# Optimization experiments

Hardware: AMD Instinct MI355X
Metric: run time of the kernel (lower is better)

The kernel has to match this reference:

```python
import jax, jax.numpy as jnp
import numpy as np

B, T, F = 4096, 256, 20
VOCAB, EMB = 1281, 4
UNITS = (64, 32, 32, 32)


def setup_inputs() -> dict:
    key = jax.random.key(0)
    ks = jax.random.split(key, 16)
    feats = jax.random.normal(ks[0], (B, T, F), jnp.float32)
    ids = jax.random.randint(ks[1], (B, T), 0, VOCAB).astype(jnp.float32)
    input_tensor = feats.at[:, :, 1].set(ids)  # column 1 = org ids
    W_emb = jax.random.normal(ks[2], (VOCAB, EMB), jnp.float32) * 0.1
    in_dims = (F - 2 + 1 + EMB,) + UNITS[:-1]  # (23, 64, 32, 32)
    out = {"input_tensor": input_tensor, "W_emb": W_emb}
    for i, (din, u) in enumerate(zip(in_dims, UNITS)):
        out[f"k{i}"] = jax.random.normal(ks[3 + 3 * i], (din, 3 * u), jnp.float32) * 0.1
        out[f"rk{i}"] = jax.random.normal(ks[4 + 3 * i], (u, 3 * u), jnp.float32) * 0.1
        out[f"b{i}"] = jnp.zeros((2, 3 * u), jnp.float32)  # [input_bias, recurrent_bias] (reset_after)
    out["Wd"] = jax.random.normal(ks[15], (UNITS[-1], 2), jnp.float32) * 0.1
    out["bd"] = jnp.zeros((2,), jnp.float32)
    return out


def _gru(h, x, k, rk, b):
    # Keras GRUCell, reset_after=True (TF2 default)
    mx = x @ k + b[0]
    mh = h @ rk + b[1]
    xz, xr, xh = jnp.split(mx, 3, axis=-1)
    hz, hr, hh = jnp.split(mh, 3, axis=-1)
    z = jax.nn.sigmoid(xz + hz)
    r = jax.nn.sigmoid(xr + hr)
    hc = jnp.tanh(xh + r * hh)
    return z * h + (1.0 - z) * hc


def reference(input_tensor, W_emb, k0, rk0, b0, k1, rk1, b1, k2, rk2, b2, k3, rk3, b3, Wd, bd):
    f0 = input_tensor[:, :, :1]                      # [B,T,1]
    ids = input_tensor[:, :, 1].astype(jnp.int32)    # [B,T]
    rest = input_tensor[:, :, 2:]                    # [B,T,F-2]
    emb = W_emb[ids]                                 # [B,T,EMB]
    x = jnp.concatenate([f0, rest, emb], axis=-1)    # [B,T,F+3]
    xs = jnp.swapaxes(x, 0, 1)                       # [T,B,F+3]
    bsz = x.shape[0]
    h_init = tuple(jnp.zeros((bsz, u), x.dtype) for u in UNITS)
    layer_params = ((k0, rk0, b0), (k1, rk1, b1), (k2, rk2, b2), (k3, rk3, b3))

    def step(carry, xt):
        hs = []
        inp = xt
        for h, (k, rk, b) in zip(carry, layer_params):
            h = _gru(h, inp, k, rk, b)
            hs.append(h)
            inp = h
        return tuple(hs), None

    hs, _ = jax.lax.scan(step, h_init, xs)
    # return_sequences + [:, -1, :] == final hidden state of last layer
    logits = hs[-1] @ Wd + bd
    return jax.nn.softmax(logits, axis=-1)
```

## Files before the change

kernel.cpp:

```cpp
#include <hip/hip_runtime.h>


typedef __attribute__((ext_vector_type(8))) __bf16 bf16x8;
typedef __attribute__((ext_vector_type(4))) float f32x4;

#define TT 256
#define FF 20
#define BT 16
#define CH 64
#define SH0 72
#define SH1 40
#define XSTR 648

__device__ __forceinline__ f32x4 mfma16(bf16x8 a, bf16x8 b, f32x4 c) {
  return __builtin_amdgcn_mfma_f32_16x16x32_bf16(a, b, c, 0, 0, 0);
}

__device__ __forceinline__ float sigm(float x) {
  return __builtin_amdgcn_rcpf(1.f + __builtin_amdgcn_exp2f(-1.44269504f * x));
}
__device__ __forceinline__ float tanh_(float x) {
  return __builtin_amdgcn_rcpf(1.f + __builtin_amdgcn_exp2f(-2.88539008f * x)) * 2.f - 1.f;
}

__device__ __forceinline__ bf16x8 bfragW(const float* W, int Kreal, int N,
                                         int ncol, int kbase) {
  bf16x8 r;
#pragma unroll
  for (int j = 0; j < 8; ++j) {
    int k = kbase + j;
    r[j] = (__bf16)(k < Kreal ? W[k * N + ncol] : 0.f);
  }
  return r;
}

__device__ __forceinline__ bf16x8 afrag(const __bf16* base, int stride, int m,
                                        int kbase) {
  return *(const bf16x8*)(base + m * stride + kbase);
}

__device__ __forceinline__ void gates(f32x4 az, f32x4 ar, f32x4 axh, f32x4 ahh,
                                      float* h, __bf16* dst, int stride, int rowq) {
#pragma unroll
  for (int r = 0; r < 4; ++r) {
    float z  = sigm(az[r]);
    float rg = sigm(ar[r]);
    float hc = tanh_(fmaf(rg, ahh[r], axh[r]));
    float hn = fmaf(z, h[r] - hc, hc);
    h[r] = hn;
    dst[(rowq + r) * stride] = (__bf16)hn;
  }
}

extern "C" __global__ void __launch_bounds__(512, 2)
gru4(const float* __restrict__ inp, const float* __restrict__ Wemb,
     const float* __restrict__ k0, const float* __restrict__ rk0, const float* __restrict__ b0,
     const float* __restrict__ k1, const float* __restrict__ rk1, const float* __restrict__ b1,
     const float* __restrict__ k2, const float* __restrict__ rk2, const float* __restrict__ b2,
     const float* __restrict__ k3, const float* __restrict__ rk3, const float* __restrict__ b3,
     const float* __restrict__ Wd, const float* __restrict__ bd,
     float* __restrict__ out)
{
  __shared__ __align__(16) __bf16 x_ch[CH * XSTR];
  __shared__ __align__(16) __bf16 h0_lds[2][BT * SH0];
  __shared__ __align__(16) __bf16 h1_lds[2][BT * SH1];
  __shared__ __align__(16) __bf16 h2_lds[2][BT * SH1];
  __shared__ __align__(16) __bf16 h3_lds[2][BT * SH1];
  __shared__ __align__(16) float h3f[BT * 32];

  const int tid  = threadIdx.x;
  const int lane = tid & 63;
  const int w    = tid >> 6;
  const int col  = lane & 15;
  const int kb   = (lane >> 4) * 8;
  const int rowq = (lane >> 4) * 4;
  const long bbase = (long)blockIdx.x * BT;
  const float* binp = inp + bbase * TT * FF;

  bf16x8 z0x, r0x, g0x, z0h0, z0h1, r0h0, r0h1, g0h0, g0h1;
  float bz0 = 0, br0 = 0, bxh0 = 0, bhh0 = 0;
  if (w < 4) {
    int u = w * 16 + col;
    z0x  = bfragW(k0, 23, 192, u, kb);
    r0x  = bfragW(k0, 23, 192, 64 + u, kb);
    g0x  = bfragW(k0, 23, 192, 128 + u, kb);
    z0h0 = bfragW(rk0, 64, 192, u, kb);
    z0h1 = bfragW(rk0, 64, 192, u, 32 + kb);
    r0h0 = bfragW(rk0, 64, 192, 64 + u, kb);
    r0h1 = bfragW(rk0, 64, 192, 64 + u, 32 + kb);
    g0h0 = bfragW(rk0, 64, 192, 128 + u, kb);
    g0h1 = bfragW(rk0, 64, 192, 128 + u, 32 + kb);
    bz0  = b0[u] + b0[192 + u];
    br0  = b0[64 + u] + b0[192 + 64 + u];
    bxh0 = b0[128 + u];
    bhh0 = b0[192 + 128 + u];
  }

  bf16x8 z1x0, z1x1, r1x0, r1x1, g1x0, g1x1, z1h, r1h, g1h;
  float bz1 = 0, br1 = 0, bxh1 = 0, bhh1 = 0;
  if (w == 4 || w == 5) {
    int u = (w - 4) * 16 + col;
    z1x0 = bfragW(k1, 64, 96, u, kb);
    z1x1 = bfragW(k1, 64, 96, u, 32 + kb);
    r1x0 = bfragW(k1, 64, 96, 32 + u, kb);
    r1x1 = bfragW(k1, 64, 96, 32 + u, 32 + kb);
    g1x0 = bfragW(k1, 64, 96, 64 + u, kb);
    g1x1 = bfragW(k1, 64, 96, 64 + u, 32 + kb);
    z1h  = bfragW(rk1, 32, 96, u, kb);
    r1h  = bfragW(rk1, 32, 96, 32 + u, kb);
    g1h  = bfragW(rk1, 32, 96, 64 + u, kb);
    bz1  = b1[u] + b1[96 + u];
    br1  = b1[32 + u] + b1[96 + 32 + u];
    bxh1 = b1[64 + u];
    bhh1 = b1[96 + 64 + u];
  }

  bf16x8 z2x, r2x, g2x, z2h, r2h, g2h;
  bf16x8 z3x, r3x, g3x, z3h, r3h, g3h;
  float bz2 = 0, br2 = 0, bxh2 = 0, bhh2 = 0;
  float bz3 = 0, br3 = 0, bxh3 = 0, bhh3 = 0;
  if (w >= 6) {
    int u = (w - 6) * 16 + col;
    z2x = bfragW(k2, 32, 96, u, kb);
    r2x = bfragW(k2, 32, 96, 32 + u, kb);
    g2x = bfragW(k2, 32, 96, 64 + u, kb);
    z2h = bfragW(rk2, 32, 96, u, kb);
    r2h = bfragW(rk2, 32, 96, 32 + u, kb);
    g2h = bfragW(rk2, 32, 96, 64 + u, kb);
    bz2  = b2[u] + b2[96 + u];
    br2  = b2[32 + u] + b2[96 + 32 + u];
    bxh2 = b2[64 + u];
    bhh2 = b2[96 + 64 + u];
    z3x = bfragW(k3, 32, 96, u, kb);
    r3x = bfragW(k3, 32, 96, 32 + u, kb);
    g3x = bfragW(k3, 32, 96, 64 + u, kb);
    z3h = bfragW(rk3, 32, 96, u, kb);
    r3h = bfragW(rk3, 32, 96, 32 + u, kb);
    g3h = bfragW(rk3, 32, 96, 64 + u, kb);
    bz3  = b3[u] + b3[96 + u];
    br3  = b3[32 + u] + b3[96 + 32 + u];
    bxh3 = b3[64 + u];
    bhh3 = b3[96 + 64 + u];
  }

  {
    __bf16* p0 = (__bf16*)h0_lds;
    for (int i = tid; i < 2 * BT * SH0; i += 512) p0[i] = (__bf16)0.f;
    __bf16* p1 = (__bf16*)h1_lds;
    __bf16* p2 = (__bf16*)h2_lds;
    __bf16* p3 = (__bf16*)h3_lds;
    for (int i = tid; i < 2 * BT * SH1; i += 512) {
      p1[i] = (__bf16)0.f; p2[i] = (__bf16)0.f; p3[i] = (__bf16)0.f;
    }
  }
  float h0r[4] = {0,0,0,0}, h1r[4] = {0,0,0,0};
  float h2r[4] = {0,0,0,0}, h3r[4] = {0,0,0,0};
  __syncthreads();

  for (int s = 0; s < TT + 3; ++s) {
    if ((s & (CH - 1)) == 0 && s < TT) {
      const int row = tid >> 5;
      const int tg  = (tid & 31) * 2;
      const float* rp = binp + ((long)row * TT + s + tg) * FF;
#pragma unroll
      for (int tt = 0; tt < 2; ++tt) {
        const float* p = rp + tt * FF;
        float4 v0 = *(const float4*)(p);
        float4 v1 = *(const float4*)(p + 4);
        float4 v2 = *(const float4*)(p + 8);
        float4 v3 = *(const float4*)(p + 12);
        float4 v4 = *(const float4*)(p + 16);
        float4 e  = *(const float4*)(Wemb + 4 * (int)v0.y);
        __bf16* d = &x_ch[(tg + tt) * XSTR + row * 40];
        bf16x8 q0 = {(__bf16)v0.x, (__bf16)v0.z, (__bf16)v0.w, (__bf16)v1.x,
                     (__bf16)v1.y, (__bf16)v1.z, (__bf16)v1.w, (__bf16)v2.x};
        bf16x8 q1 = {(__bf16)v2.y, (__bf16)v2.z, (__bf16)v2.w, (__bf16)v3.x,
                     (__bf16)v3.y, (__bf16)v3.z, (__bf16)v3.w, (__bf16)v4.x};
        bf16x8 q2 = {(__bf16)v4.y, (__bf16)v4.z, (__bf16)v4.w, (__bf16)e.x,
                     (__bf16)e.y,  (__bf16)e.z,  (__bf16)e.w,  (__bf16)0.f};
        bf16x8 q3 = {(__bf16)0.f, (__bf16)0.f, (__bf16)0.f, (__bf16)0.f,
                     (__bf16)0.f, (__bf16)0.f, (__bf16)0.f, (__bf16)0.f};
        *(bf16x8*)(d)      = q0;
        *(bf16x8*)(d + 8)  = q1;
        *(bf16x8*)(d + 16) = q2;
        *(bf16x8*)(d + 24) = q3;
      }
      __syncthreads();
    }

    const int pb = (s + 1) & 1;
    const int qb = s & 1;

    if (w < 4) {
      if (s < TT) {
        const int tl = s & (CH - 1);
        bf16x8 ax = *(const bf16x8*)(&x_ch[tl * XSTR + col * 40 + kb]);
        bf16x8 a0 = afrag(h0_lds[pb], SH0, col, kb);
        bf16x8 a1 = afrag(h0_lds[pb], SH0, col, 32 + kb);
        f32x4 az  = {bz0, bz0, bz0, bz0};
        f32x4 ar  = {br0, br0, br0, br0};
        f32x4 axh = {bxh0, bxh0, bxh0, bxh0};
        f32x4 ahh = {bhh0, bhh0, bhh0, bhh0};
        az  = mfma16(ax, z0x, az);  az  = mfma16(a0, z0h0, az);  az = mfma16(a1, z0h1, az);
        ar  = mfma16(ax, r0x, ar);  ar  = mfma16(a0, r0h0, ar);  ar = mfma16(a1, r0h1, ar);
        axh = mfma16(ax, g0x, axh);
        ahh = mfma16(a0, g0h0, ahh); ahh = mfma16(a1, g0h1, ahh);
        gates(az, ar, axh, ahh, h0r, &h0_lds[qb][w * 16 + col], SH0, rowq);
      }
    } else if (w < 6) {
      if (s >= 1 && s <= TT) {
        bf16x8 ax0 = afrag(h0_lds[pb], SH0, col, kb);
        bf16x8 ax1 = afrag(h0_lds[pb], SH0, col, 32 + kb);
        bf16x8 ah  = afrag(h1_lds[pb], SH1, col, kb);
        f32x4 az  = {bz1, bz1, bz1, bz1};
        f32x4 ar  = {br1, br1, br1, br1};
        f32x4 axh = {bxh1, bxh1, bxh1, bxh1};
        f32x4 ahh = {bhh1, bhh1, bhh1, bhh1};
        az  = mfma16(ax0, z1x0, az);  az  = mfma16(ax1, z1x1, az);  az = mfma16(ah, z1h, az);
        ar  = mfma16(ax0, r1x0, ar);  ar  = mfma16(ax1, r1x1, ar);  ar = mfma16(ah, r1h, ar);
        axh = mfma16(ax0, g1x0, axh); axh = mfma16(ax1, g1x1, axh);
        ahh = mfma16(ah, g1h, ahh);
        gates(az, ar, axh, ahh, h1r, &h1_lds[qb][(w - 4) * 16 + col], SH1, rowq);
      }
    } else {
      bf16x8 a1 = afrag(h1_lds[pb], SH1, col, kb);
      bf16x8 a2 = afrag(h2_lds[pb], SH1, col, kb);
      bf16x8 a3 = afrag(h3_lds[pb], SH1, col, kb);
      if (s >= 2 && s <= TT + 1) {
        f32x4 az  = {bz2, bz2, bz2, bz2};
        f32x4 ar  = {br2, br2, br2, br2};
        f32x4 axh = {bxh2, bxh2, bxh2, bxh2};
        f32x4 ahh = {bhh2, bhh2, bhh2, bhh2};
        az  = mfma16(a1, z2x, az);  az = mfma16(a2, z2h, az);
        ar  = mfma16(a1, r2x, ar);  ar = mfma16(a2, r2h, ar);
        axh = mfma16(a1, g2x, axh);
        ahh = mfma16(a2, g2h, ahh);
        gates(az, ar, axh, ahh, h2r, &h2_lds[qb][(w - 6) * 16 + col], SH1, rowq);
      }
      if (s >= 3) {
        f32x4 az  = {bz3, bz3, bz3, bz3};
        f32x4 ar  = {br3, br3, br3, br3};
        f32x4 axh = {bxh3, bxh3, bxh3, bxh3};
        f32x4 ahh = {bhh3, bhh3, bhh3, bhh3};
        az  = mfma16(a2, z3x, az);  az = mfma16(a3, z3h, az);
        ar  = mfma16(a2, r3x, ar);  ar = mfma16(a3, r3h, ar);
        axh = mfma16(a2, g3x, axh);
        ahh = mfma16(a3, g3h, ahh);
        gates(az, ar, axh, ahh, h3r, &h3_lds[qb][(w - 6) * 16 + col], SH1, rowq);
      }
    }

    __syncthreads();
  }

  if (w >= 6) {
#pragma unroll
    for (int r = 0; r < 4; ++r)
      h3f[(rowq + r) * 32 + (w - 6) * 16 + col] = h3r[r];
  }
  __syncthreads();

  if (tid < BT) {
    float l0 = bd[0], l1 = bd[1];
#pragma unroll
    for (int u = 0; u < 32; ++u) {
      float h = h3f[tid * 32 + u];
      l0 = fmaf(h, Wd[2 * u], l0);
      l1 = fmaf(h, Wd[2 * u + 1], l1);
    }
    float m = fmaxf(l0, l1);
    float e0 = __builtin_amdgcn_exp2f((l0 - m) * 1.44269504f);
    float e1 = __builtin_amdgcn_exp2f((l1 - m) * 1.44269504f);
    float inv = 1.f / (e0 + e1);
    out[(bbase + tid) * 2 + 0] = e0 * inv;
    out[(bbase + tid) * 2 + 1] = e1 * inv;
  }
}

extern "C" void kernel_launch(void* const* d_in, const int* in_sizes, int n_in,
                              void* d_out, int out_size, void* d_ws, size_t ws_size,
                              hipStream_t stream) {
  const float* inp  = (const float*)d_in[0];
  const float* Wemb = (const float*)d_in[1];
  const float* k0   = (const float*)d_in[2];
  const float* rk0  = (const float*)d_in[3];
  const float* b0   = (const float*)d_in[4];
  const float* k1   = (const float*)d_in[5];
  const float* rk1  = (const float*)d_in[6];
  const float* b1   = (const float*)d_in[7];
  const float* k2   = (const float*)d_in[8];
  const float* rk2  = (const float*)d_in[9];
  const float* b2   = (const float*)d_in[10];
  const float* k3   = (const float*)d_in[11];
  const float* rk3  = (const float*)d_in[12];
  const float* b3   = (const float*)d_in[13];
  const float* Wd   = (const float*)d_in[14];
  const float* bd   = (const float*)d_in[15];
  float* out = (float*)d_out;

  const int Btot = in_sizes[0] / (TT * FF);
  dim3 grid(Btot / BT);
  gru4<<<grid, 512, 0, stream>>>(inp, Wemb, k0, rk0, b0, k1, rk1, b1,
                                 k2, rk2, b2, k3, rk3, b3, Wd, bd, out);
}
```

Baseline: 365.6 us.

## Rebalance GRU layer work across twelve waves with uniform per-wave step code

Grows the block from 8 to 12 waves. Layers 2 and 3 now get their own waves instead of one wave doing both, and layer 0 is split across six waves: some duplicate the MFMA work and each computes only half of the gate rows. Every wave runs the same generic MFMA plus gate sequence, chosen by per-wave pointers and flags, which shortens the longest wave's critical path per timestep. The cost is more waves per block, a changed occupancy target (launch bounds 768 threads, 3 blocks), redundant MFMAs on the layer-0 waves, and branchy generic code with possibly wasted zero-weight MFMAs.

```diff
diff --git a/kernel.cpp b/kernel.cpp
--- a/kernel.cpp
+++ b/kernel.cpp
@@ -11,6 +11,7 @@
 #define SH0 72
 #define SH1 40
 #define XSTR 648
+#define NTHR 768
 
 __device__ __forceinline__ f32x4 mfma16(bf16x8 a, bf16x8 b, f32x4 c) {
   return __builtin_amdgcn_mfma_f32_16x16x32_bf16(a, b, c, 0, 0, 0);
@@ -34,25 +35,7 @@
   return r;
 }
 
-__device__ __forceinline__ bf16x8 afrag(const __bf16* base, int stride, int m,
-                                        int kbase) {
-  return *(const bf16x8*)(base + m * stride + kbase);
-}
-
-__device__ __forceinline__ void gates(f32x4 az, f32x4 ar, f32x4 axh, f32x4 ahh,
-                                      float* h, __bf16* dst, int stride, int rowq) {
-#pragma unroll
-  for (int r = 0; r < 4; ++r) {
-    float z  = sigm(az[r]);
-    float rg = sigm(ar[r]);
-    float hc = tanh_(fmaf(rg, ahh[r], axh[r]));
-    float hn = fmaf(z, h[r] - hc, hc);
-    h[r] = hn;
-    dst[(rowq + r) * stride] = (__bf16)hn;
-  }
-}
-
-extern "C" __global__ void __launch_bounds__(512, 2)
+extern "C" __global__ void __launch_bounds__(NTHR, 3)
 gru4(const float* __restrict__ inp, const float* __restrict__ Wemb,
      const float* __restrict__ k0, const float* __restrict__ rk0, const float* __restrict__ b0,
      const float* __restrict__ k1, const float* __restrict__ rk1, const float* __restrict__ b1,
@@ -77,186 +60,192 @@
   const long bbase = (long)blockIdx.x * BT;
   const float* binp = inp + bbase * TT * FF;
 
-  bf16x8 z0x, r0x, g0x, z0h0, z0h1, r0h0, r0h1, g0h0, g0h1;
-  float bz0 = 0, br0 = 0, bxh0 = 0, bhh0 = 0;
-  if (w < 4) {
-    int u = w * 16 + col;
-    z0x  = bfragW(k0, 23, 192, u, kb);
-    r0x  = bfragW(k0, 23, 192, 64 + u, kb);
-    g0x  = bfragW(k0, 23, 192, 128 + u, kb);
-    z0h0 = bfragW(rk0, 64, 192, u, kb);
-    z0h1 = bfragW(rk0, 64, 192, u, 32 + kb);
-    r0h0 = bfragW(rk0, 64, 192, 64 + u, kb);
-    r0h1 = bfragW(rk0, 64, 192, 64 + u, 32 + kb);
-    g0h0 = bfragW(rk0, 64, 192, 128 + u, kb);
-    g0h1 = bfragW(rk0, 64, 192, 128 + u, 32 + kb);
-    bz0  = b0[u] + b0[192 + u];
-    br0  = b0[64 + u] + b0[192 + 64 + u];
-    bxh0 = b0[128 + u];
-    bhh0 = b0[192 + 128 + u];
-  }
-
-  bf16x8 z1x0, z1x1, r1x0, r1x1, g1x0, g1x1, z1h, r1h, g1h;
-  float bz1 = 0, br1 = 0, bxh1 = 0, bhh1 = 0;
-  if (w == 4 || w == 5) {
-    int u = (w - 4) * 16 + col;
-    z1x0 = bfragW(k1, 64, 96, u, kb);
-    z1x1 = bfragW(k1, 64, 96, u, 32 + kb);
-    r1x0 = bfragW(k1, 64, 96, 32 + u, kb);
-    r1x1 = bfragW(k1, 64, 96, 32 + u, 32 + kb);
-    g1x0 = bfragW(k1, 64, 96, 64 + u, kb);
-    g1x1 = bfragW(k1, 64, 96, 64 + u, 32 + kb);
-    z1h  = bfragW(rk1, 32, 96, u, kb);
-    r1h  = bfragW(rk1, 32, 96, 32 + u, kb);
-    g1h  = bfragW(rk1, 32, 96, 64 + u, kb);
-    bz1  = b1[u] + b1[96 + u];
-    br1  = b1[32 + u] + b1[96 + 32 + u];
-    bxh1 = b1[64 + u];
-    bhh1 = b1[96 + 64 + u];
-  }
-
-  bf16x8 z2x, r2x, g2x, z2h, r2h, g2h;
-  bf16x8 z3x, r3x, g3x, z3h, r3h, g3h;
-  float bz2 = 0, br2 = 0, bxh2 = 0, bhh2 = 0;
-  float bz3 = 0, br3 = 0, bxh3 = 0, bhh3 = 0;
-  if (w >= 6) {
-    int u = (w - 6) * 16 + col;
-    z2x = bfragW(k2, 32, 96, u, kb);
-    r2x = bfragW(k2, 32, 96, 32 + u, kb);
-    g2x = bfragW(k2, 32, 96, 64 + u, kb);
-    z2h = bfragW(rk2, 32, 96, u, kb);
-    r2h = bfragW(rk2, 32, 96, 32 + u, kb);
-    g2h = bfragW(rk2, 32, 96, 64 + u, kb);
-    bz2  = b2[u] + b2[96 + u];
-    br2  = b2[32 + u] + b2[96 + 32 + u];
-    bxh2 = b2[64 + u];
-    bhh2 = b2[96 + 64 + u];
-    z3x = bfragW(k3, 32, 96, u, kb);
-    r3x = bfragW(k3, 32, 96, 32 + u, kb);
-    g3x = bfragW(k3, 32, 96, 64 + u, kb);
-    z3h = bfragW(rk3, 32, 96, u, kb);
-    r3h = bfragW(rk3, 32, 96, 32 + u, kb);
-    g3h = bfragW(rk3, 32, 96, 64 + u, kb);
-    bz3  = b3[u] + b3[96 + u];
-    br3  = b3[32 + u] + b3[96 + 32 + u];
-    bxh3 = b3[64 + u];
-    bhh3 = b3[96 + 64 + u];
-  }
+  bf16x8 zf;
+#pragma unroll
+  for (int j = 0; j < 8; ++j) zf[j] = (__bf16)0.f;
+
+  bf16x8 Wz0 = zf, Wz1 = zf, Wz2 = zf;
+  bf16x8 Wr0 = zf, Wr1 = zf, Wr2 = zf;
+  bf16x8 Wgx0 = zf, Wgx1 = zf, Wgx2 = zf;
+  bf16x8 Wgh0 = zf, Wgh1 = zf, Wgh2 = zf;
+  float bz = 0.f, br = 0.f, bxh = 0.f, bhh = 0.f;
+  const __bf16 *A0b = x_ch, *A1b = x_ch, *A2b = x_ch;
+  int D0 = 0, D1 = 0, D2 = 0;
+  __bf16* Wwr0 = (__bf16*)h3f;
+  int WD = 0, wstride = SH1;
+  int lay = 0;
+  bool doLo = false, doHi = false, threeA = false;
+
+  if (w < 6) {
+    lay = 0; threeA = true;
+    const int sl = (w < 4) ? (w >> 1) : (w - 2);
+    doLo = (w >= 4) || ((w & 1) == 0);
+    doHi = (w >= 4) || ((w & 1) == 1);
+    const int u = sl * 16 + col;
+    Wz0 = bfragW(k0, 23, 192, u, kb);
+    Wz1 = bfragW(rk0, 64, 192, u, kb);
+    Wz2 = bfragW(rk0, 64, 192, u, 32 + kb);
+    Wr0 = bfragW(k0, 23, 192, 64 + u, kb);
+    Wr1 = bfragW(rk0, 64, 192, 64 + u, kb);
+    Wr2 = bfragW(rk0, 64, 192, 64 + u, 32 + kb);
+    Wgx0 = bfragW(k0, 23, 192, 128 + u, kb);
+    Wgh1 = bfragW(rk0, 64, 192, 128 + u, kb);
+    Wgh2 = bfragW(rk0, 64, 192, 128 + u, 32 + kb);
+    bz  = b0[u] + b0[192 + u];
+    br  = b0[64 + u] + b0[192 + 64 + u];
+    bxh = b0[128 + u];
+    bhh = b0[192 + 128 + u];
+    A1b = &h0_lds[0][col * SH0 + kb];      D1 = BT * SH0;
+    A2b = &h0_lds[0][col * SH0 + 32 + kb]; D2 = BT * SH0;
+    Wwr0 = &h0_lds[0][rowq * SH0 + sl * 16 + col];
+    WD = BT * SH0; wstride = SH0;
+  } else if (w < 8) {
+    lay = 1; threeA = true; doLo = doHi = true;
+    const int u = (w - 6) * 16 + col;
+    Wz0 = bfragW(k1, 64, 96, u, kb);
+    Wz1 = bfragW(k1, 64, 96, u, 32 + kb);
+    Wz2 = bfragW(rk1, 32, 96, u, kb);
+    Wr0 = bfragW(k1, 64, 96, 32 + u, kb);
+    Wr1 = bfragW(k1, 64, 96, 32 + u, 32 + kb);
+    Wr2 = bfragW(rk1, 32, 96, 32 + u, kb);
+    Wgx0 = bfragW(k1, 64, 96, 64 + u, kb);
+    Wgx1 = bfragW(k1, 64, 96, 64 + u, 32 + kb);
+    Wgh2 = bfragW(rk1, 32, 96, 64 + u, kb);
+    bz  = b1[u] + b1[96 + u];
+    br  = b1[32 + u] + b1[96 + 32 + u];
+    bxh = b1[64 + u];
+    bhh = b1[96 + 64 + u];
+    A0b = &h0_lds[0][col * SH0 + kb];      D0 = BT * SH0;
+    A1b = &h0_lds[0][col * SH0 + 32 + kb]; D1 = BT * SH0;
+    A2b = &h1_lds[0][col * SH1 + kb];      D2 = BT * SH1;
+    Wwr0 = &h1_lds[0][rowq * SH1 + (w - 6) * 16 + col];
+    WD = BT * SH1; wstride = SH1;
+  } else if (w < 10) {
+    lay = 2; threeA = false; doLo = doHi = true;
+    const int u = (w - 8) * 16 + col;
+    Wz0 = bfragW(k2, 32, 96, u, kb);
+    Wz1 = bfragW(rk2, 32, 96, u, kb);
+    Wr0 = bfragW(k2, 32, 96, 32 + u, kb);
+    Wr1 = bfragW(rk2, 32, 96, 32 + u, kb);
+    Wgx0 = bfragW(k2, 32, 96, 64 + u, kb);
+    Wgh1 = bfragW(rk2, 32, 96, 64 + u, kb);
+    bz  = b2[u] + b2[96 + u];
+    br  = b2[32 + u] + b2[96 + 32 + u];
+    bxh = b2[64 + u];
+    bhh = b2[96 + 64 + u];
+    A0b = &h1_lds[0][col * SH1 + kb]; D0 = BT * SH1;
+    A1b = &h2_lds[0][col * SH1 + kb]; D1 = BT * SH1;
+    A2b = A1b; D2 = D1;
+    Wwr0 = &h2_lds[0][rowq * SH1 + (w - 8) * 16 + col];
+    WD = BT * SH1; wstride = SH1;
+  } else {
+    lay = 3; threeA = false; doLo = doHi = true;
+    const int u = (w - 10) * 16 + col;
+    Wz0 = bfragW(k3, 32, 96, u, kb);
+    Wz1 = bfragW(rk3, 32, 96, u, kb);
+    Wr0 = bfragW(k3, 32, 96, 32 + u, kb);
+    Wr1 = bfragW(rk3, 32, 96, 32 + u, kb);
+    Wgx0 = bfragW(k3, 32, 96, 64 + u, kb);
+    Wgh1 = bfragW(rk3, 32, 96, 64 + u, kb);
+    bz  = b3[u] + b3[96 + u];
+    br  = b3[32 + u] + b3[96 + 32 + u];
+    bxh = b3[64 + u];
+    bhh = b3[96 + 64 + u];
+    A0b = &h2_lds[0][col * SH1 + kb]; D0 = BT * SH1;
+    A1b = &h3_lds[0][col * SH1 + kb]; D1 = BT * SH1;
+    A2b = A1b; D2 = D1;
+    Wwr0 = &h3_lds[0][rowq * SH1 + (w - 10) * 16 + col];
+    WD = BT * SH1; wstride = SH1;
+  }
+
+  const __bf16* xb = &x_ch[col * 40 + kb];
 
   {
     __bf16* p0 = (__bf16*)h0_lds;
-    for (int i = tid; i < 2 * BT * SH0; i += 512) p0[i] = (__bf16)0.f;
+    for (int i = tid; i < 2 * BT * SH0; i += NTHR) p0[i] = (__bf16)0.f;
     __bf16* p1 = (__bf16*)h1_lds;
     __bf16* p2 = (__bf16*)h2_lds;
     __bf16* p3 = (__bf16*)h3_lds;
-    for (int i = tid; i < 2 * BT * SH1; i += 512) {
+    for (int i = tid; i < 2 * BT * SH1; i += NTHR) {
       p1[i] = (__bf16)0.f; p2[i] = (__bf16)0.f; p3[i] = (__bf16)0.f;
     }
   }
-  float h0r[4] = {0,0,0,0}, h1r[4] = {0,0,0,0};
-  float h2r[4] = {0,0,0,0}, h3r[4] = {0,0,0,0};
+  float hreg[4] = {0.f, 0.f, 0.f, 0.f};
   __syncthreads();
 
   for (int s = 0; s < TT + 3; ++s) {
     if ((s & (CH - 1)) == 0 && s < TT) {
-      const int row = tid >> 5;
-      const int tg  = (tid & 31) * 2;
-      const float* rp = binp + ((long)row * TT + s + tg) * FF;
-#pragma unroll
-      for (int tt = 0; tt < 2; ++tt) {
-        const float* p = rp + tt * FF;
+      for (int idx = tid; idx < BT * CH; idx += NTHR) {
+        const int row = idx >> 6;
+        const int tg  = idx & (CH - 1);
+        const float* p = binp + ((long)row * TT + s + tg) * FF;
         float4 v0 = *(const float4*)(p);
         float4 v1 = *(const float4*)(p + 4);
         float4 v2 = *(const float4*)(p + 8);
         float4 v3 = *(const float4*)(p + 12);
         float4 v4 = *(const float4*)(p + 16);
         float4 e  = *(const float4*)(Wemb + 4 * (int)v0.y);
-        __bf16* d = &x_ch[(tg + tt) * XSTR + row * 40];
+        __bf16* d = &x_ch[tg * XSTR + row * 40];
         bf16x8 q0 = {(__bf16)v0.x, (__bf16)v0.z, (__bf16)v0.w, (__bf16)v1.x,
                      (__bf16)v1.y, (__bf16)v1.z, (__bf16)v1.w, (__bf16)v2.x};
         bf16x8 q1 = {(__bf16)v2.y, (__bf16)v2.z, (__bf16)v2.w, (__bf16)v3.x,
                      (__bf16)v3.y, (__bf16)v3.z, (__bf16)v3.w, (__bf16)v4.x};
         bf16x8 q2 = {(__bf16)v4.y, (__bf16)v4.z, (__bf16)v4.w, (__bf16)e.x,
                      (__bf16)e.y,  (__bf16)e.z,  (__bf16)e.w,  (__bf16)0.f};
-        bf16x8 q3 = {(__bf16)0.f, (__bf16)0.f, (__bf16)0.f, (__bf16)0.f,
-                     (__bf16)0.f, (__bf16)0.f, (__bf16)0.f, (__bf16)0.f};
         *(bf16x8*)(d)      = q0;
         *(bf16x8*)(d + 8)  = q1;
         *(bf16x8*)(d + 16) = q2;
-        *(bf16x8*)(d + 24) = q3;
+        *(bf16x8*)(d + 24) = zf;
       }
       __syncthreads();
     }
 
     const int pb = (s + 1) & 1;
     const int qb = s & 1;
-
-    if (w < 4) {
-      if (s < TT) {
-        const int tl = s & (CH - 1);
-        bf16x8 ax = *(const bf16x8*)(&x_ch[tl * XSTR + col * 40 + kb]);
-        bf16x8 a0 = afrag(h0_lds[pb], SH0, col, kb);
-        bf16x8 a1 = afrag(h0_lds[pb], SH0, col, 32 + kb);
-        f32x4 az  = {bz0, bz0, bz0, bz0};
-        f32x4 ar  = {br0, br0, br0, br0};
-        f32x4 axh = {bxh0, bxh0, bxh0, bxh0};
-        f32x4 ahh = {bhh0, bhh0, bhh0, bhh0};
-        az  = mfma16(ax, z0x, az);  az  = mfma16(a0, z0h0, az);  az = mfma16(a1, z0h1, az);
-        ar  = mfma16(ax, r0x, ar);  ar  = mfma16(a0, r0h0, ar);  ar = mfma16(a1, r0h1, ar);
-        axh = mfma16(ax, g0x, axh);
-        ahh = mfma16(a0, g0h0, ahh); ahh = mfma16(a1, g0h1, ahh);
-        gates(az, ar, axh, ahh, h0r, &h0_lds[qb][w * 16 + col], SH0, rowq);
+    const int t  = s - lay;
+
+    if (t >= 0 && t < TT) {
+      const __bf16* a0p = (lay == 0) ? (xb + (s & (CH - 1)) * XSTR)
+                                     : (A0b + pb * D0);
+      bf16x8 A0 = *(const bf16x8*)a0p;
+      bf16x8 A1 = *(const bf16x8*)(A1b + pb * D1);
+      f32x4 az  = {bz, bz, bz, bz};
+      f32x4 ar  = {br, br, br, br};
+      f32x4 axh = {bxh, bxh, bxh, bxh};
+      f32x4 ahh = {bhh, bhh, bhh, bhh};
+      az  = mfma16(A0, Wz0, az);   az  = mfma16(A1, Wz1, az);
+      ar  = mfma16(A0, Wr0, ar);   ar  = mfma16(A1, Wr1, ar);
+      axh = mfma16(A0, Wgx0, axh); axh = mfma16(A1, Wgx1, axh);
+      ahh = mfma16(A0, Wgh0, ahh); ahh = mfma16(A1, Wgh1, ahh);
+      if (threeA) {
+        bf16x8 A2 = *(const bf16x8*)(A2b + pb * D2);
+        az  = mfma16(A2, Wz2, az);
+        ar  = mfma16(A2, Wr2, ar);
+        axh = mfma16(A2, Wgx2, axh);
+        ahh = mfma16(A2, Wgh2, ahh);
       }
-    } else if (w < 6) {
-      if (s >= 1 && s <= TT) {
-        bf16x8 ax0 = afrag(h0_lds[pb], SH0, col, kb);
-        bf16x8 ax1 = afrag(h0_lds[pb], SH0, col, 32 + kb);
-        bf16x8 ah  = afrag(h1_lds[pb], SH1, col, kb);
-        f32x4 az  = {bz1, bz1, bz1, bz1};
-        f32x4 ar  = {br1, br1, br1, br1};
-        f32x4 axh = {bxh1, bxh1, bxh1, bxh1};
-        f32x4 ahh = {bhh1, bhh1, bhh1, bhh1};
-        az  = mfma16(ax0, z1x0, az);  az  = mfma16(ax1, z1x1, az);  az = mfma16(ah, z1h, az);
-        ar  = mfma16(ax0, r1x0, ar);  ar  = mfma16(ax1, r1x1, ar);  ar = mfma16(ah, r1h, ar);
-        axh = mfma16(ax0, g1x0, axh); axh = mfma16(ax1, g1x1, axh);
-        ahh = mfma16(ah, g1h, ahh);
-        gates(az, ar, axh, ahh, h1r, &h1_lds[qb][(w - 4) * 16 + col], SH1, rowq);
-      }
-    } else {
-      bf16x8 a1 = afrag(h1_lds[pb], SH1, col, kb);
-      bf16x8 a2 = afrag(h2_lds[pb], SH1, col, kb);
-      bf16x8 a3 = afrag(h3_lds[pb], SH1, col, kb);
-      if (s >= 2 && s <= TT + 1) {
-        f32x4 az  = {bz2, bz2, bz2, bz2};
-        f32x4 ar  = {br2, br2, br2, br2};
-        f32x4 axh = {bxh2, bxh2, bxh2, bxh2};
-        f32x4 ahh = {bhh2, bhh2, bhh2, bhh2};
-        az  = mfma16(a1, z2x, az);  az = mfma16(a2, z2h, az);
-        ar  = mfma16(a1, r2x, ar);  ar = mfma16(a2, r2h, ar);
-        axh = mfma16(a1, g2x, axh);
-        ahh = mfma16(a2, g2h, ahh);
-        gates(az, ar, axh, ahh, h2r, &h2_lds[qb][(w - 6) * 16 + col], SH1, rowq);
-      }
-      if (s >= 3) {
-        f32x4 az  = {bz3, bz3, bz3, bz3};
-        f32x4 ar  = {br3, br3, br3, br3};
-        f32x4 axh = {bxh3, bxh3, bxh3, bxh3};
-        f32x4 ahh = {bhh3, bhh3, bhh3, bhh3};
-        az  = mfma16(a2, z3x, az);  az = mfma16(a3, z3h, az);
-        ar  = mfma16(a2, r3x, ar);  ar = mfma16(a3, r3h, ar);
-        axh = mfma16(a2, g3x, axh);
-        ahh = mfma16(a3, g3h, ahh);
-        gates(az, ar, axh, ahh, h3r, &h3_lds[qb][(w - 6) * 16 + col], SH1, rowq);
-      }
+      __bf16* wr = Wwr0 + qb * WD;
+
+#define GATE(r) { \
+        float z  = sigm(az[r]); \
+        float rg = sigm(ar[r]); \
+        float hc = tanh_(fmaf(rg, ahh[r], axh[r])); \
+        float hn = fmaf(z, hreg[r] - hc, hc); \
+        hreg[r] = hn; \
+        wr[(r) * wstride] = (__bf16)hn; }
+
+      if (doLo) { GATE(0); GATE(1); }
+      if (doHi) { GATE(2); GATE(3); }
+#undef GATE
     }
 
     __syncthreads();
   }
 
-  if (w >= 6) {
+  if (w >= 10) {
 #pragma unroll
     for (int r = 0; r < 4; ++r)
-      h3f[(rowq + r) * 32 + (w - 6) * 16 + col] = h3r[r];
+      h3f[(rowq + r) * 32 + (w - 10) * 16 + col] = hreg[r];
   }
   __syncthreads();
 
@@ -300,6 +289,6 @@
 
   const int Btot = in_sizes[0] / (TT * FF);
   dim3 grid(Btot / BT);
-  gru4<<<grid, 512, 0, stream>>>(inp, Wemb, k0, rk0, b0, k1, rk1, b1,
-                                 k2, rk2, b2, k3, rk3, b3, Wd, bd, out);
-}
+  gru4<<<grid, NTHR, 0, stream>>>(inp, Wemb, k0, rk0, b0, k1, rk1, b1,
+                                  k2, rk2, b2, k3, rk3, b3, Wd, bd, out);
+}
```

New measurement: 342.9 us. -6.2%, faster.
